# Kernel optimization log

Measured on AMD Instinct MI355X. Metric: run time of the kernel, lower is better.

Reference implementation:

```python
import jax, jax.numpy as jnp
import numpy as np

B, P, D, L, K = 8192, 4096, 1024, 5, 5
EPS = 1e-8  # torch.cosine_similarity default eps


def setup_inputs() -> dict:
    key = jax.random.key(0)
    k1, k2, k3 = jax.random.split(key, 3)
    x = jax.random.normal(k1, (B, 1, D), dtype=jnp.float32)
    # parameters initialized uniform(0, 0.01) as in the torch module
    keys = jax.random.uniform(k2, (P, D), dtype=jnp.float32, minval=0.0, maxval=0.01)
    values = jax.random.uniform(k3, (P, L, D), dtype=jnp.float32, minval=0.0, maxval=0.01)
    return {"x": x, "keys": keys, "values": values}


def reference(x, keys, values):
    xq = x[:, 0, :]                                   # [B, D]
    # cosine similarity: dot / max(||x||*||k||, eps)
    dot = jnp.einsum("bd,pd->bp", xq, keys)           # [B, P]
    xn = jnp.linalg.norm(xq, axis=-1, keepdims=True)  # [B, 1]
    kn = jnp.linalg.norm(keys, axis=-1)               # [P]
    cos = dot / jnp.maximum(xn * kn[None, :], EPS)
    dist = 1.0 - cos                                  # [B, P]
    # topk smallest distances (largest=False) -> negate and take top_k
    neg_sel, idx = jax.lax.top_k(-dist, K)            # [B, K]
    sel_dist = -neg_sel
    key_loss = sel_dist.mean()
    prompts = values[idx].reshape(xq.shape[0], K * L, D)  # [B, K*L, D]
    return prompts, key_loss
```

## Files before the change

kernel.cpp:

```cpp
#include <hip/hip_runtime.h>
#include <stdint.h>

#define BDIM 8192
#define PDIM 4096
#define DDIM 1024
#define LDIM 5
#define KSEL 5
#define EPSV 1e-8f

#define BM 64
#define BN 256
#define BK 16
#define SPLITS 8
#define CPS (PDIM / SPLITS)
#define NTILES (CPS / BN)

__device__ __forceinline__ void insert5(unsigned long long t[5], unsigned long long c) {
    if (c < t[4]) {
        if (c < t[3]) { t[4] = t[3];
            if (c < t[2]) { t[3] = t[2];
                if (c < t[1]) { t[2] = t[1];
                    if (c < t[0]) { t[1] = t[0]; t[0] = c; }
                    else t[1] = c;
                } else t[2] = c;
            } else t[3] = c;
        } else t[4] = c;
    }
}

__global__ __launch_bounds__(256) void norms_kernel(
        const float* __restrict__ x, const float* __restrict__ keys,
        float* __restrict__ xn, float* __restrict__ kn) {
    int b = blockIdx.x;
    const float* src; float* dst;
    if (b < PDIM) { src = keys + (size_t)b * DDIM; dst = kn + b; }
    else          { src = x + (size_t)(b - PDIM) * DDIM; dst = xn + (b - PDIM); }
    float4 v = ((const float4*)src)[threadIdx.x];
    float s = v.x*v.x + v.y*v.y + v.z*v.z + v.w*v.w;
    #pragma unroll
    for (int m = 32; m; m >>= 1) s += __shfl_xor(s, m, 64);
    __shared__ float red[4];
    if ((threadIdx.x & 63) == 0) red[threadIdx.x >> 6] = s;
    __syncthreads();
    if (threadIdx.x == 0) *dst = sqrtf(red[0] + red[1] + red[2] + red[3]);
}

__global__ __launch_bounds__(256) void score_topk_kernel(
        const float* __restrict__ x, const float* __restrict__ keys,
        const float* __restrict__ xn, const float* __restrict__ kn,
        unsigned long long* __restrict__ part) {
    __shared__ float Xs[BK][BM + 4];
    __shared__ float Ks[BK][BN + 8];

    const int tid = threadIdx.x;
    const int tx = tid & 31, ty = tid >> 5;
    const int row0 = blockIdx.x * BM;
    const int split = blockIdx.y;
    const int rb = ty * 8, cb = tx * 8;

    unsigned long long t5[8][5];
    #pragma unroll
    for (int i = 0; i < 8; ++i)
        #pragma unroll
        for (int k = 0; k < 5; ++k) t5[i][k] = ~0ULL;

    for (int tile = 0; tile < NTILES; ++tile) {
        const int c0 = split * CPS + tile * BN;
        float acc[8][8];
        #pragma unroll
        for (int i = 0; i < 8; ++i)
            #pragma unroll
            for (int j = 0; j < 8; ++j) acc[i][j] = 0.f;

        for (int kc = 0; kc < DDIM; kc += BK) {
            const int xr = tid >> 2, xk = (tid & 3) << 2;
            float4 xv = *(const float4*)&x[(size_t)(row0 + xr) * DDIM + kc + xk];
            float4 kv[4];
            #pragma unroll
            for (int i2 = 0; i2 < 4; ++i2) {
                int idx = tid + i2 * 256;
                int kr = idx >> 2, kk = (idx & 3) << 2;
                kv[i2] = *(const float4*)&keys[(size_t)(c0 + kr) * DDIM + kc + kk];
            }
            __syncthreads();
            Xs[xk + 0][xr] = xv.x; Xs[xk + 1][xr] = xv.y;
            Xs[xk + 2][xr] = xv.z; Xs[xk + 3][xr] = xv.w;
            #pragma unroll
            for (int i2 = 0; i2 < 4; ++i2) {
                int idx = tid + i2 * 256;
                int kr = idx >> 2, kk = (idx & 3) << 2;
                Ks[kk + 0][kr] = kv[i2].x; Ks[kk + 1][kr] = kv[i2].y;
                Ks[kk + 2][kr] = kv[i2].z; Ks[kk + 3][kr] = kv[i2].w;
            }
            __syncthreads();

            #pragma unroll
            for (int k = 0; k < BK; ++k) {
                float a[8], bq[8];
                *(float4*)&a[0]  = *(const float4*)&Xs[k][rb];
                *(float4*)&a[4]  = *(const float4*)&Xs[k][rb + 4];
                *(float4*)&bq[0] = *(const float4*)&Ks[k][cb];
                *(float4*)&bq[4] = *(const float4*)&Ks[k][cb + 4];
                #pragma unroll
                for (int i = 0; i < 8; ++i)
                    #pragma unroll
                    for (int j = 0; j < 8; ++j)
                        acc[i][j] = fmaf(a[i], bq[j], acc[i][j]);
            }
        }

        float kn8[8], xn8[8];
        #pragma unroll
        for (int j = 0; j < 8; ++j) kn8[j] = kn[c0 + cb + j];
        #pragma unroll
        for (int i = 0; i < 8; ++i) xn8[i] = xn[row0 + rb + i];
        #pragma unroll
        for (int i = 0; i < 8; ++i) {
            #pragma unroll
            for (int j = 0; j < 8; ++j) {
                float denom = fmaxf(xn8[i] * kn8[j], EPSV);
                float dist = 1.0f - acc[i][j] / denom;
                unsigned long long c =
                    ((unsigned long long)__float_as_uint(dist) << 32) |
                    (unsigned long long)(unsigned)(c0 + cb + j);
                insert5(t5[i], c);
            }
        }
    }

    #pragma unroll
    for (int m = 1; m <= 16; m <<= 1) {
        #pragma unroll
        for (int i = 0; i < 8; ++i) {
            unsigned long long o[5];
            #pragma unroll
            for (int k = 0; k < 5; ++k) o[k] = __shfl_xor(t5[i][k], m, 64);
            #pragma unroll
            for (int k = 0; k < 5; ++k) insert5(t5[i], o[k]);
        }
    }
    if (tx == 0) {
        #pragma unroll
        for (int i = 0; i < 8; ++i) {
            size_t base = ((size_t)(row0 + rb + i) * SPLITS + split) * 5;
            #pragma unroll
            for (int k = 0; k < 5; ++k) part[base + k] = t5[i][k];
        }
    }
}

__global__ __launch_bounds__(256) void gather_kernel(
        const unsigned long long* __restrict__ part,
        const float* __restrict__ values,
        float* __restrict__ out, float* __restrict__ row_loss) {
    const int row = blockIdx.x;
    __shared__ int sidx[KSEL];
    if (threadIdx.x == 0) {
        unsigned long long t[5] = {~0ULL, ~0ULL, ~0ULL, ~0ULL, ~0ULL};
        const unsigned long long* p = part + (size_t)row * SPLITS * 5;
        #pragma unroll
        for (int i = 0; i < SPLITS * 5; ++i) insert5(t, p[i]);
        float s = 0.f;
        #pragma unroll
        for (int k = 0; k < KSEL; ++k) {
            sidx[k] = (int)(t[k] & 0xFFFFFFFFULL);
            s += __uint_as_float((unsigned)(t[k] >> 32));
        }
        row_loss[row] = s;
    }
    __syncthreads();
    float4* dst = (float4*)(out + (size_t)row * (KSEL * LDIM * DDIM));
    #pragma unroll
    for (int k = 0; k < KSEL; ++k) {
        const float4* src = (const float4*)(values + (size_t)sidx[k] * (LDIM * DDIM));
        float4* dstk = dst + k * (LDIM * DDIM / 4);
        for (int o = threadIdx.x; o < LDIM * DDIM / 4; o += 256) dstk[o] = src[o];
    }
}

__global__ __launch_bounds__(256) void loss_reduce_kernel(
        const float* __restrict__ row_loss, float* __restrict__ out_loss) {
    float s = 0.f;
    for (int i = threadIdx.x; i < BDIM; i += 256) s += row_loss[i];
    #pragma unroll
    for (int m = 32; m; m >>= 1) s += __shfl_xor(s, m, 64);
    __shared__ float red[4];
    if ((threadIdx.x & 63) == 0) red[threadIdx.x >> 6] = s;
    __syncthreads();
    if (threadIdx.x == 0)
        *out_loss = (red[0] + red[1] + red[2] + red[3]) * (1.0f / (BDIM * KSEL));
}

extern "C" void kernel_launch(void* const* d_in, const int* in_sizes, int n_in,
                              void* d_out, int out_size, void* d_ws, size_t ws_size,
                              hipStream_t stream) {
    const float* x      = (const float*)d_in[0];
    const float* keys   = (const float*)d_in[1];
    const float* values = (const float*)d_in[2];
    float* out = (float*)d_out;

    unsigned long long* part = (unsigned long long*)d_ws;
    float* kn       = (float*)((char*)d_ws + 2621440);
    float* xn       = (float*)((char*)d_ws + 2621440 + 16384);
    float* row_loss = (float*)((char*)d_ws + 2621440 + 16384 + 32768);

    norms_kernel<<<PDIM + BDIM, 256, 0, stream>>>(x, keys, xn, kn);
    score_topk_kernel<<<dim3(BDIM / BM, SPLITS), 256, 0, stream>>>(x, keys, xn, kn, part);
    gather_kernel<<<BDIM, 256, 0, stream>>>(part, values, out, row_loss);
    loss_reduce_kernel<<<1, 256, 0, stream>>>(row_loss, out + (size_t)BDIM * KSEL * LDIM * DDIM);
}
```

Measured before the change: 2.193 ms.

## Replace FP32 FMA scoring with split-bf16 MFMA GEMM plus FP32 rescoring of candidates

Each input is converted to a hi/lo bf16 pair so the dot products run on MFMA 16x16x32 bf16 instructions. The three cross terms (hi*hi, lo*hi, hi*lo) are packed into a K=3072 product, and tiles are staged through LDS with direct global-to-LDS loads. Each 128x128 tile writes a per-row top-8 to a partial buffer. A new select kernel merges these candidates and recomputes the top 8 distances exactly in FP32 before picking the final top-5. The bf16 copies and the partial buffer live in the output buffer as scratch until the gather kernel overwrites it. The risk is that the approximate scores could drop a true top-5 key that the top-8 rescoring fails to recover.

```diff
diff --git a/kernel.cpp b/kernel.cpp
--- a/kernel.cpp
+++ b/kernel.cpp
@@ -8,14 +8,19 @@
 #define KSEL 5
 #define EPSV 1e-8f
 
-#define BM 64
-#define BN 256
-#define BK 16
-#define SPLITS 8
-#define CPS (PDIM / SPLITS)
-#define NTILES (CPS / BN)
-
-__device__ __forceinline__ void insert5(unsigned long long t[5], unsigned long long c) {
+#define KSPL 2048
+#define KPROD 3072
+#define GBK 32
+#define NCB (PDIM / 128)
+#define NCAND (NCB * 8)
+
+typedef unsigned long long u64;
+typedef __bf16 bf16x8 __attribute__((ext_vector_type(8)));
+typedef float f32x4 __attribute__((ext_vector_type(4)));
+
+struct __align__(8) bf4 { __bf16 h[4]; };
+
+__device__ __forceinline__ void insert5(u64 t[5], u64 c) {
     if (c < t[4]) {
         if (c < t[3]) { t[4] = t[3];
             if (c < t[2]) { t[3] = t[2];
@@ -28,153 +33,235 @@
     }
 }
 
-__global__ __launch_bounds__(256) void norms_kernel(
+__device__ __forceinline__ void insert8(u64 t[8], u64 c) {
+    if (c < t[7]) {
+        t[7] = c;
+        #pragma unroll
+        for (int i = 7; i > 0; --i) {
+            u64 a = t[i - 1], b = t[i];
+            u64 lo = b < a ? b : a;
+            u64 hi = b < a ? a : b;
+            t[i - 1] = lo; t[i] = hi;
+        }
+    }
+}
+
+__device__ __forceinline__ void gload16(const void* g, void* l) {
+    __builtin_amdgcn_global_load_lds(
+        (const __attribute__((address_space(1))) uint32_t*)g,
+        (__attribute__((address_space(3))) uint32_t*)(uintptr_t)l,
+        16, 0, 0);
+}
+
+__global__ __launch_bounds__(256) void convert_split_kernel(
         const float* __restrict__ x, const float* __restrict__ keys,
+        __bf16* __restrict__ Xc, __bf16* __restrict__ Kc,
         float* __restrict__ xn, float* __restrict__ kn) {
     int b = blockIdx.x;
-    const float* src; float* dst;
-    if (b < PDIM) { src = keys + (size_t)b * DDIM; dst = kn + b; }
-    else          { src = x + (size_t)(b - PDIM) * DDIM; dst = xn + (b - PDIM); }
+    const float* src; __bf16* dst; float* nrm;
+    if (b < PDIM) { src = keys + (size_t)b * DDIM; dst = Kc + (size_t)b * KSPL; nrm = kn + b; }
+    else { int r = b - PDIM; src = x + (size_t)r * DDIM; dst = Xc + (size_t)r * KSPL; nrm = xn + r; }
     float4 v = ((const float4*)src)[threadIdx.x];
-    float s = v.x*v.x + v.y*v.y + v.z*v.z + v.w*v.w;
+    float f[4] = {v.x, v.y, v.z, v.w};
+    bf4 hi, lo;
+    #pragma unroll
+    for (int i = 0; i < 4; ++i) {
+        __bf16 h = (__bf16)f[i];
+        hi.h[i] = h;
+        lo.h[i] = (__bf16)(f[i] - (float)h);
+    }
+    *(bf4*)(dst + (size_t)threadIdx.x * 4) = hi;
+    *(bf4*)(dst + 1024 + (size_t)threadIdx.x * 4) = lo;
+    float s = v.x * v.x + v.y * v.y + v.z * v.z + v.w * v.w;
     #pragma unroll
     for (int m = 32; m; m >>= 1) s += __shfl_xor(s, m, 64);
     __shared__ float red[4];
     if ((threadIdx.x & 63) == 0) red[threadIdx.x >> 6] = s;
     __syncthreads();
-    if (threadIdx.x == 0) *dst = sqrtf(red[0] + red[1] + red[2] + red[3]);
-}
-
-__global__ __launch_bounds__(256) void score_topk_kernel(
+    if (threadIdx.x == 0) *nrm = sqrtf(red[0] + red[1] + red[2] + red[3]);
+}
+
+__global__ __launch_bounds__(256, 2) void gemm_topk_kernel(
+        const __bf16* __restrict__ Xc, const __bf16* __restrict__ Kc,
+        const float* __restrict__ xn, const float* __restrict__ kn,
+        u64* __restrict__ part) {
+    __shared__ union {
+        struct { __bf16 A[128 * GBK]; __bf16 B[128 * GBK]; } g;
+        float slab[64 * 128];
+    } sm;
+
+    const int tid = threadIdx.x;
+    const int lane = tid & 63;
+    const int w = tid >> 6, wr = w >> 1, wc = w & 1;
+    const int row0 = blockIdx.y * 128;
+    const int col0 = blockIdx.x * 128;
+    const int fr = lane & 15, fq = lane >> 4;
+
+    f32x4 acc[4][4];
+    #pragma unroll
+    for (int m = 0; m < 4; ++m)
+        #pragma unroll
+        for (int n = 0; n < 4; ++n)
+            #pragma unroll
+            for (int r = 0; r < 4; ++r) acc[m][n][r] = 0.f;
+
+    for (int kc = 0; kc < KPROD; kc += GBK) {
+        const int asrc = (kc < 2048) ? kc : kc - 2048;
+        const int bsrc = (kc < 1024) ? kc : kc - 1024;
+        __syncthreads();
+        #pragma unroll
+        for (int i = 0; i < 2; ++i) {
+            int chunk = i * 256 + tid;
+            int r = chunk >> 2, k8 = (chunk & 3) << 3;
+            gload16(Xc + (size_t)(row0 + r) * KSPL + asrc + k8, sm.g.A + chunk * 8);
+            gload16(Kc + (size_t)(col0 + r) * KSPL + bsrc + k8, sm.g.B + chunk * 8);
+        }
+        __syncthreads();
+        bf16x8 af[4], bb[4];
+        #pragma unroll
+        for (int m = 0; m < 4; ++m)
+            af[m] = *(const bf16x8*)&sm.g.A[(wr * 64 + m * 16 + fr) * GBK + fq * 8];
+        #pragma unroll
+        for (int n = 0; n < 4; ++n)
+            bb[n] = *(const bf16x8*)&sm.g.B[(wc * 64 + n * 16 + fr) * GBK + fq * 8];
+        #pragma unroll
+        for (int m = 0; m < 4; ++m)
+            #pragma unroll
+            for (int n = 0; n < 4; ++n)
+                acc[m][n] = __builtin_amdgcn_mfma_f32_16x16x32_bf16(af[m], bb[n], acc[m][n], 0, 0, 0);
+    }
+
+    float knv[4], xnv[4][4];
+    #pragma unroll
+    for (int n = 0; n < 4; ++n) knv[n] = kn[col0 + wc * 64 + n * 16 + fr];
+    #pragma unroll
+    for (int m = 0; m < 4; ++m)
+        #pragma unroll
+        for (int r = 0; r < 4; ++r)
+            xnv[m][r] = xn[row0 + wr * 64 + m * 16 + fq * 4 + r];
+
+    #pragma unroll
+    for (int mh = 0; mh < 2; ++mh) {
+        __syncthreads();
+        #pragma unroll
+        for (int ml = 0; ml < 2; ++ml) {
+            int m = mh * 2 + ml;
+            #pragma unroll
+            for (int n = 0; n < 4; ++n) {
+                #pragma unroll
+                for (int r = 0; r < 4; ++r) {
+                    float denom = fmaxf(xnv[m][r] * knv[n], EPSV);
+                    float dist = 1.0f - acc[m][n][r] / denom;
+                    int sr = wr * 32 + ml * 16 + fq * 4 + r;
+                    int sc = wc * 64 + n * 16 + fr;
+                    sm.slab[sr * 128 + sc] = dist;
+                }
+            }
+        }
+        __syncthreads();
+        const int sr = tid >> 2, seg = tid & 3;
+        const int grow = row0 + (sr >> 5) * 64 + mh * 32 + (sr & 31);
+        u64 t8[8];
+        #pragma unroll
+        for (int k = 0; k < 8; ++k) t8[k] = ~0ULL;
+        #pragma unroll
+        for (int j = 0; j < 32; ++j) {
+            int c = seg * 32 + ((j + sr + seg * 8) & 31);
+            float d = sm.slab[sr * 128 + c];
+            insert8(t8, ((u64)__float_as_uint(d) << 32) | (unsigned)(col0 + c));
+        }
+        #pragma unroll
+        for (int mm = 1; mm <= 2; mm <<= 1) {
+            u64 o[8];
+            #pragma unroll
+            for (int k = 0; k < 8; ++k) o[k] = __shfl_xor(t8[k], mm, 64);
+            #pragma unroll
+            for (int k = 0; k < 8; ++k) insert8(t8, o[k]);
+        }
+        if (seg == 0) {
+            u64* p = part + ((size_t)grow * NCB + blockIdx.x) * 8;
+            #pragma unroll
+            for (int k = 0; k < 8; ++k) p[k] = t8[k];
+        }
+    }
+}
+
+__global__ __launch_bounds__(256) void select_kernel(
+        const u64* __restrict__ part,
         const float* __restrict__ x, const float* __restrict__ keys,
         const float* __restrict__ xn, const float* __restrict__ kn,
-        unsigned long long* __restrict__ part) {
-    __shared__ float Xs[BK][BM + 4];
-    __shared__ float Ks[BK][BN + 8];
-
+        int* __restrict__ sidx, float* __restrict__ row_loss) {
+    const int row = blockIdx.x;
     const int tid = threadIdx.x;
-    const int tx = tid & 31, ty = tid >> 5;
-    const int row0 = blockIdx.x * BM;
-    const int split = blockIdx.y;
-    const int rb = ty * 8, cb = tx * 8;
-
-    unsigned long long t5[8][5];
-    #pragma unroll
-    for (int i = 0; i < 8; ++i)
-        #pragma unroll
-        for (int k = 0; k < 5; ++k) t5[i][k] = ~0ULL;
-
-    for (int tile = 0; tile < NTILES; ++tile) {
-        const int c0 = split * CPS + tile * BN;
-        float acc[8][8];
-        #pragma unroll
-        for (int i = 0; i < 8; ++i)
-            #pragma unroll
-            for (int j = 0; j < 8; ++j) acc[i][j] = 0.f;
-
-        for (int kc = 0; kc < DDIM; kc += BK) {
-            const int xr = tid >> 2, xk = (tid & 3) << 2;
-            float4 xv = *(const float4*)&x[(size_t)(row0 + xr) * DDIM + kc + xk];
-            float4 kv[4];
-            #pragma unroll
-            for (int i2 = 0; i2 < 4; ++i2) {
-                int idx = tid + i2 * 256;
-                int kr = idx >> 2, kk = (idx & 3) << 2;
-                kv[i2] = *(const float4*)&keys[(size_t)(c0 + kr) * DDIM + kc + kk];
-            }
-            __syncthreads();
-            Xs[xk + 0][xr] = xv.x; Xs[xk + 1][xr] = xv.y;
-            Xs[xk + 2][xr] = xv.z; Xs[xk + 3][xr] = xv.w;
-            #pragma unroll
-            for (int i2 = 0; i2 < 4; ++i2) {
-                int idx = tid + i2 * 256;
-                int kr = idx >> 2, kk = (idx & 3) << 2;
-                Ks[kk + 0][kr] = kv[i2].x; Ks[kk + 1][kr] = kv[i2].y;
-                Ks[kk + 2][kr] = kv[i2].z; Ks[kk + 3][kr] = kv[i2].w;
-            }
-            __syncthreads();
-
-            #pragma unroll
-            for (int k = 0; k < BK; ++k) {
-                float a[8], bq[8];
-                *(float4*)&a[0]  = *(const float4*)&Xs[k][rb];
-                *(float4*)&a[4]  = *(const float4*)&Xs[k][rb + 4];
-                *(float4*)&bq[0] = *(const float4*)&Ks[k][cb];
-                *(float4*)&bq[4] = *(const float4*)&Ks[k][cb + 4];
-                #pragma unroll
-                for (int i = 0; i < 8; ++i)
-                    #pragma unroll
-                    for (int j = 0; j < 8; ++j)
-                        acc[i][j] = fmaf(a[i], bq[j], acc[i][j]);
-            }
-        }
-
-        float kn8[8], xn8[8];
-        #pragma unroll
-        for (int j = 0; j < 8; ++j) kn8[j] = kn[c0 + cb + j];
-        #pragma unroll
-        for (int i = 0; i < 8; ++i) xn8[i] = xn[row0 + rb + i];
-        #pragma unroll
-        for (int i = 0; i < 8; ++i) {
-            #pragma unroll
-            for (int j = 0; j < 8; ++j) {
-                float denom = fmaxf(xn8[i] * kn8[j], EPSV);
-                float dist = 1.0f - acc[i][j] / denom;
-                unsigned long long c =
-                    ((unsigned long long)__float_as_uint(dist) << 32) |
-                    (unsigned long long)(unsigned)(c0 + cb + j);
-                insert5(t5[i], c);
-            }
-        }
-    }
-
-    #pragma unroll
-    for (int m = 1; m <= 16; m <<= 1) {
-        #pragma unroll
-        for (int i = 0; i < 8; ++i) {
-            unsigned long long o[5];
-            #pragma unroll
-            for (int k = 0; k < 5; ++k) o[k] = __shfl_xor(t5[i][k], m, 64);
-            #pragma unroll
-            for (int k = 0; k < 5; ++k) insert5(t5[i], o[k]);
-        }
-    }
-    if (tx == 0) {
-        #pragma unroll
-        for (int i = 0; i < 8; ++i) {
-            size_t base = ((size_t)(row0 + rb + i) * SPLITS + split) * 5;
-            #pragma unroll
-            for (int k = 0; k < 5; ++k) part[base + k] = t5[i][k];
-        }
+    __shared__ u64 cand8[8];
+    __shared__ u64 ex8[8];
+
+    if (tid < 64) {
+        u64 t8[8];
+        #pragma unroll
+        for (int k = 0; k < 8; ++k) t8[k] = ~0ULL;
+        const u64* p = part + (size_t)row * NCAND;
+        #pragma unroll
+        for (int i = 0; i < 4; ++i) insert8(t8, p[tid + i * 64]);
+        #pragma unroll
+        for (int mm = 1; mm <= 32; mm <<= 1) {
+            u64 o[8];
+            #pragma unroll
+            for (int k = 0; k < 8; ++k) o[k] = __shfl_xor(t8[k], mm, 64);
+            #pragma unroll
+            for (int k = 0; k < 8; ++k) insert8(t8, o[k]);
+        }
+        if (tid == 0) {
+            #pragma unroll
+            for (int k = 0; k < 8; ++k) cand8[k] = t8[k];
+        }
+    }
+    __syncthreads();
+
+    const int w = tid >> 6, lane = tid & 63;
+    const float* xr = x + (size_t)row * DDIM;
+    #pragma unroll
+    for (int ci = 0; ci < 2; ++ci) {
+        int cidx = (int)(cand8[w * 2 + ci] & 0xFFFFFFFFULL);
+        const float* kr = keys + (size_t)cidx * DDIM;
+        float s = 0.f;
+        #pragma unroll
+        for (int j = 0; j < DDIM / 64; ++j)
+            s += xr[j * 64 + lane] * kr[j * 64 + lane];
+        #pragma unroll
+        for (int mm = 32; mm; mm >>= 1) s += __shfl_xor(s, mm, 64);
+        if (lane == 0) {
+            float denom = fmaxf(xn[row] * kn[cidx], EPSV);
+            float dist = 1.0f - s / denom;
+            ex8[w * 2 + ci] = ((u64)__float_as_uint(dist) << 32) | (unsigned)cidx;
+        }
+    }
+    __syncthreads();
+    if (tid == 0) {
+        u64 t[5] = {~0ULL, ~0ULL, ~0ULL, ~0ULL, ~0ULL};
+        #pragma unroll
+        for (int i = 0; i < 8; ++i) insert5(t, ex8[i]);
+        float ls = 0.f;
+        #pragma unroll
+        for (int k = 0; k < KSEL; ++k) {
+            sidx[row * KSEL + k] = (int)(t[k] & 0xFFFFFFFFULL);
+            ls += __uint_as_float((unsigned)(t[k] >> 32));
+        }
+        row_loss[row] = ls;
     }
 }
 
 __global__ __launch_bounds__(256) void gather_kernel(
-        const unsigned long long* __restrict__ part,
-        const float* __restrict__ values,
-        float* __restrict__ out, float* __restrict__ row_loss) {
+        const int* __restrict__ sidx, const float* __restrict__ values,
+        float* __restrict__ out) {
     const int row = blockIdx.x;
-    __shared__ int sidx[KSEL];
-    if (threadIdx.x == 0) {
-        unsigned long long t[5] = {~0ULL, ~0ULL, ~0ULL, ~0ULL, ~0ULL};
-        const unsigned long long* p = part + (size_t)row * SPLITS * 5;
-        #pragma unroll
-        for (int i = 0; i < SPLITS * 5; ++i) insert5(t, p[i]);
-        float s = 0.f;
-        #pragma unroll
-        for (int k = 0; k < KSEL; ++k) {
-            sidx[k] = (int)(t[k] & 0xFFFFFFFFULL);
-            s += __uint_as_float((unsigned)(t[k] >> 32));
-        }
-        row_loss[row] = s;
-    }
-    __syncthreads();
+    const int tid = threadIdx.x;
     float4* dst = (float4*)(out + (size_t)row * (KSEL * LDIM * DDIM));
     #pragma unroll
     for (int k = 0; k < KSEL; ++k) {
-        const float4* src = (const float4*)(values + (size_t)sidx[k] * (LDIM * DDIM));
+        const float4* src = (const float4*)(values + (size_t)sidx[row * KSEL + k] * (LDIM * DDIM));
         float4* dstk = dst + k * (LDIM * DDIM / 4);
-        for (int o = threadIdx.x; o < LDIM * DDIM / 4; o += 256) dstk[o] = src[o];
+        for (int o = tid; o < LDIM * DDIM / 4; o += 256) dstk[o] = src[o];
     }
 }
 
@@ -199,13 +286,20 @@
     const float* values = (const float*)d_in[2];
     float* out = (float*)d_out;
 
-    unsigned long long* part = (unsigned long long*)d_ws;
-    float* kn       = (float*)((char*)d_ws + 2621440);
-    float* xn       = (float*)((char*)d_ws + 2621440 + 16384);
-    float* row_loss = (float*)((char*)d_ws + 2621440 + 16384 + 32768);
-
-    norms_kernel<<<PDIM + BDIM, 256, 0, stream>>>(x, keys, xn, kn);
-    score_topk_kernel<<<dim3(BDIM / BM, SPLITS), 256, 0, stream>>>(x, keys, xn, kn, part);
-    gather_kernel<<<BDIM, 256, 0, stream>>>(part, values, out, row_loss);
+    char* big = (char*)d_out;
+    __bf16* Xc  = (__bf16*)big;
+    __bf16* Kc  = (__bf16*)(big + 33554432);
+    u64*   part = (u64*)  (big + 50331648);
+
+    char* ws = (char*)d_ws;
+    float* xn       = (float*)ws;
+    float* kn       = (float*)(ws + 32768);
+    float* row_loss = (float*)(ws + 49152);
+    int*   sidx     = (int*)  (ws + 81920);
+
+    convert_split_kernel<<<PDIM + BDIM, 256, 0, stream>>>(x, keys, Xc, Kc, xn, kn);
+    gemm_topk_kernel<<<dim3(NCB, BDIM / 128), 256, 0, stream>>>(Xc, Kc, xn, kn, part);
+    select_kernel<<<BDIM, 256, 0, stream>>>(part, x, keys, xn, kn, sidx, row_loss);
+    gather_kernel<<<BDIM, 256, 0, stream>>>(sidx, values, out);
     loss_reduce_kernel<<<1, 256, 0, stream>>>(row_loss, out + (size_t)BDIM * KSEL * LDIM * DDIM);
 }
```

New measurement: 1.864 ms. -15.0%, faster.
